# Optimization experiments

Measured on AMD Instinct MI355X. Metric: run time of the kernel, lower is better.

## Reference

```python
import jax, jax.numpy as jnp
import numpy as np

N_NODES = 50000
N_EDGES = 800000
D_IN = 128
D_HID = 128
D_OUT = 2


def setup_inputs() -> dict:
    key = jax.random.key(0)
    ks = jax.random.split(key, 8)
    x = jax.random.normal(ks[0], (N_NODES, D_IN), dtype=jnp.float32)
    edge_index = jax.random.randint(ks[1], (2, N_EDGES), 0, N_NODES, dtype=jnp.int64)
    s = 0.05
    W1_l = jax.random.normal(ks[2], (D_HID, D_IN), dtype=jnp.float32) * s
    W1_r = jax.random.normal(ks[3], (D_HID, D_IN), dtype=jnp.float32) * s
    b1 = jax.random.normal(ks[4], (D_HID,), dtype=jnp.float32) * s
    W2_l = jax.random.normal(ks[5], (D_OUT, D_HID), dtype=jnp.float32) * s
    W2_r = jax.random.normal(ks[6], (D_OUT, D_HID), dtype=jnp.float32) * s
    b2 = jax.random.normal(ks[7], (D_OUT,), dtype=jnp.float32) * s
    return {"x": x, "edge_index": edge_index, "W1_l": W1_l, "W1_r": W1_r,
            "b1": b1, "W2_l": W2_l, "W2_r": W2_r, "b2": b2}


def _sage_conv(x, src, dst, W_l, W_r, b):
    # mean-aggregate neighbor features: gather from src, scatter-sum to dst
    n = x.shape[0]
    msg = x[src]                                            # [E, d]
    agg = jax.ops.segment_sum(msg, dst, num_segments=n)      # [n, d]
    cnt = jax.ops.segment_sum(jnp.ones((src.shape[0],), x.dtype), dst,
                              num_segments=n)
    agg = agg / jnp.maximum(cnt, 1.0)[:, None]
    # lin_l(aggregated) + lin_r(self) + bias  (PyG SAGEConv with root_weight)
    return agg @ W_l.T + x @ W_r.T + b


def reference(x, edge_index, W1_l, W1_r, b1, W2_l, W2_r, b2):
    src, dst = edge_index[0], edge_index[1]
    h = _sage_conv(x, src, dst, W1_l, W1_r, b1)
    h = jax.nn.relu(h)
    out = _sage_conv(h, src, dst, W2_l, W2_r, b2)
    return out
```

## Files before the change

kernel.cpp:

```cpp
#include <hip/hip_runtime.h>

#define N_NODES 50000
#define N_EDGES 800000

typedef __bf16 bf16_8 __attribute__((ext_vector_type(8)));
typedef float  f32_4  __attribute__((ext_vector_type(4)));


__global__ void prep_kernel(const float* __restrict__ W1l, const float* __restrict__ W1r,
                            __bf16* __restrict__ Wt, const float* __restrict__ x,
                            __bf16* __restrict__ xb, int4* __restrict__ deg_p4) {
    int b = blockIdx.x;
    if (b < 3125) {
        int t = b * 256 + threadIdx.x;
        int node = t >> 4, c8 = t & 15;
        const float4* xp = (const float4*)(x + node * 128 + c8 * 8);
        float4 v0 = xp[0], v1 = xp[1];
        bf16_8 o;
        o[0] = (__bf16)v0.x; o[1] = (__bf16)v0.y; o[2] = (__bf16)v0.z; o[3] = (__bf16)v0.w;
        o[4] = (__bf16)v1.x; o[5] = (__bf16)v1.y; o[6] = (__bf16)v1.z; o[7] = (__bf16)v1.w;
        *(bf16_8*)(xb + node * 128 + c8 * 8) = o;
    } else if (b < 3253) {
        int t = (b - 3125) * 256 + threadIdx.x;
        int n = t >> 8, k = t & 255;
        float v = (k < 128) ? W1l[n * 128 + k] : W1r[n * 128 + (k - 128)];
        Wt[t] = (__bf16)v;
    } else {
        int t = (b - 3253) * 256 + threadIdx.x;
        if (t < 200000) deg_p4[t] = make_int4(0, 0, 0, 0);
    }
}

__global__ void deg_pos_kernel(const int* __restrict__ dst, int* __restrict__ deg_p,
                               int* __restrict__ edge_pos) {
    int e = blockIdx.x * 256 + threadIdx.x;
    edge_pos[e] = atomicAdd(&deg_p[dst[e] * 16], 1);
}

__global__ void scan_block_kernel(const int* __restrict__ deg_p, int* __restrict__ rowptr,
                                  int* __restrict__ degc, int* __restrict__ bsum) {
    __shared__ int s[256];
    int i = blockIdx.x * 256 + threadIdx.x;
    int v = (i < N_NODES) ? deg_p[i * 16] : 0;
    if (i < N_NODES) degc[i] = v;
    s[threadIdx.x] = v;
    __syncthreads();
    #pragma unroll
    for (int off = 1; off < 256; off <<= 1) {
        int t = (threadIdx.x >= off) ? s[threadIdx.x - off] : 0;
        __syncthreads();
        s[threadIdx.x] += t;
        __syncthreads();
    }
    if (i < N_NODES) rowptr[i] = s[threadIdx.x] - v;
    if (threadIdx.x == 255) bsum[blockIdx.x] = s[255];
}

__global__ void scan_bsum_kernel(int* __restrict__ bsum) {
    __shared__ int s[256];
    int v = (threadIdx.x < 196) ? bsum[threadIdx.x] : 0;
    s[threadIdx.x] = v;
    __syncthreads();
    #pragma unroll
    for (int off = 1; off < 256; off <<= 1) {
        int t = (threadIdx.x >= off) ? s[threadIdx.x - off] : 0;
        __syncthreads();
        s[threadIdx.x] += t;
        __syncthreads();
    }
    if (threadIdx.x < 196) bsum[threadIdx.x] = s[threadIdx.x] - v;
}

__global__ void fill_csr_kernel(const int* __restrict__ src, const int* __restrict__ dst,
                                const int* __restrict__ rowptr, const int* __restrict__ bsum,
                                const int* __restrict__ edge_pos, int* __restrict__ csr) {
    int e = blockIdx.x * 256 + threadIdx.x;
    int d = dst[e];
    csr[rowptr[d] + bsum[d >> 8] + edge_pos[e]] = src[e];
}

__global__ __launch_bounds__(256) void agg_kernel(
    const int* __restrict__ rowptr, const int* __restrict__ bsum,
    const int* __restrict__ degc, const int* __restrict__ csr,
    const __bf16* __restrict__ xb, __bf16* __restrict__ aggb)
{
    int t = blockIdx.x * 256 + threadIdx.x;
    int node = t >> 4, c8 = t & 15;
    int beg = rowptr[node] + bsum[node >> 8], n = degc[node];
    float acc[8] = {};
    int j = 0;
    for (; j + 2 <= n; j += 2) {
        int s0 = csr[beg + j], s1 = csr[beg + j + 1];
        bf16_8 v0 = *(const bf16_8*)(xb + s0 * 128 + c8 * 8);
        bf16_8 v1 = *(const bf16_8*)(xb + s1 * 128 + c8 * 8);
        #pragma unroll
        for (int u = 0; u < 8; ++u) acc[u] += (float)v0[u] + (float)v1[u];
    }
    if (j < n) {
        int s0 = csr[beg + j];
        bf16_8 v0 = *(const bf16_8*)(xb + s0 * 128 + c8 * 8);
        #pragma unroll
        for (int u = 0; u < 8; ++u) acc[u] += (float)v0[u];
    }
    float inv = 1.0f / fmaxf((float)n, 1.0f);
    bf16_8 o;
    #pragma unroll
    for (int u = 0; u < 8; ++u) o[u] = (__bf16)(acc[u] * inv);
    *(bf16_8*)(aggb + node * 128 + c8 * 8) = o;
}

#define LDA 264
__global__ __launch_bounds__(256) void gemm_fused_kernel(
    const __bf16* __restrict__ aggb, const __bf16* __restrict__ xb,
    const __bf16* __restrict__ Wt, const float* __restrict__ b1,
    const float* __restrict__ W2l, const float* __restrict__ W2r,
    float* __restrict__ y, float* __restrict__ z)
{
    __shared__ __bf16 As[64 * LDA];
    const int i0 = blockIdx.x * 64;
    const int tid = threadIdx.x;

    #pragma unroll
    for (int s = 0; s < 8; ++s) {
        int v = tid + s * 256;
        int row = v >> 5, c8 = v & 31;
        int gi = i0 + row;
        bf16_8 val = {};
        if (gi < N_NODES) {
            val = (c8 < 16) ? *(const bf16_8*)(aggb + gi * 128 + c8 * 8)
                            : *(const bf16_8*)(xb + gi * 128 + (c8 - 16) * 8);
        }
        *(bf16_8*)(&As[row * LDA + c8 * 8]) = val;
    }
    __syncthreads();

    const int wv = tid >> 6, lane = tid & 63;
    const int m0 = wv * 16;
    const int mr = lane & 15, q = lane >> 4;

    f32_4 acc[8];
    #pragma unroll
    for (int nt = 0; nt < 8; ++nt) acc[nt] = (f32_4){0.f, 0.f, 0.f, 0.f};

    #pragma unroll
    for (int ks = 0; ks < 8; ++ks) {
        bf16_8 a = *(const bf16_8*)(&As[(m0 + mr) * LDA + ks * 32 + q * 8]);
        #pragma unroll
        for (int nt = 0; nt < 8; ++nt) {
            bf16_8 b = *(const bf16_8*)(Wt + (nt * 16 + mr) * 256 + ks * 32 + q * 8);
            acc[nt] = __builtin_amdgcn_mfma_f32_16x16x32_bf16(a, b, acc[nt], 0, 0, 0);
        }
    }

    float py0[4] = {}, py1[4] = {}, pz0[4] = {}, pz1[4] = {};
    #pragma unroll
    for (int nt = 0; nt < 8; ++nt) {
        int col = nt * 16 + mr;
        float bb  = b1[col];
        float wl0 = W2l[col], wl1 = W2l[128 + col];
        float wr0 = W2r[col], wr1 = W2r[128 + col];
        #pragma unroll
        for (int r = 0; r < 4; ++r) {
            float hv = fmaxf(acc[nt][r] + bb, 0.f);
            py0[r] += hv * wl0; py1[r] += hv * wl1;
            pz0[r] += hv * wr0; pz1[r] += hv * wr1;
        }
    }
    #pragma unroll
    for (int off = 1; off < 16; off <<= 1) {
        #pragma unroll
        for (int r = 0; r < 4; ++r) {
            py0[r] += __shfl_xor(py0[r], off);
            py1[r] += __shfl_xor(py1[r], off);
            pz0[r] += __shfl_xor(pz0[r], off);
            pz1[r] += __shfl_xor(pz1[r], off);
        }
    }
    if (mr < 4) {
        int r = mr;
        int row = i0 + m0 + q * 4 + r;
        if (row < N_NODES) {
            ((float2*)y)[row] = make_float2(py0[r], py1[r]);
            ((float2*)z)[row] = make_float2(pz0[r], pz1[r]);
        }
    }
}

__global__ void final_kernel(const int* __restrict__ rowptr, const int* __restrict__ bsum,
                             const int* __restrict__ degc, const int* __restrict__ csr,
                             const float* __restrict__ y, const float* __restrict__ z,
                             const float* __restrict__ b2, float* __restrict__ out) {
    int t = blockIdx.x * 256 + threadIdx.x;
    if (t >= 2 * N_NODES) return;
    int node = t >> 1, c = t & 1;
    int beg = rowptr[node] + bsum[node >> 8], n = degc[node];
    float acc = 0.f;
    for (int j = 0; j < n; ++j) acc += y[csr[beg + j] * 2 + c];
    out[t] = acc / fmaxf((float)n, 1.0f) + z[t] + b2[c];
}

extern "C" void kernel_launch(void* const* d_in, const int* in_sizes, int n_in,
                              void* d_out, int out_size, void* d_ws, size_t ws_size,
                              hipStream_t stream) {
    const float* x   = (const float*)d_in[0];
    const int*   ei  = (const int*)  d_in[1];
    const float* W1l = (const float*)d_in[2];
    const float* W1r = (const float*)d_in[3];
    const float* b1  = (const float*)d_in[4];
    const float* W2l = (const float*)d_in[5];
    const float* W2r = (const float*)d_in[6];
    const float* b2  = (const float*)d_in[7];
    float* out = (float*)d_out;
    const int* src = ei;
    const int* dst = ei + N_EDGES;

    char* ws = (char*)d_ws;
    int*    deg_p    = (int*)   (ws + 0);
    int*    edge_pos = (int*)   (ws + 3200000);
    int*    rowptr   = (int*)   (ws + 6400000);
    int*    degc     = (int*)   (ws + 6600192);
    int*    bsum     = (int*)   (ws + 6800384);
    int*    csr      = (int*)   (ws + 6801408);
    __bf16* xb       = (__bf16*)(ws + 10001408);
    __bf16* aggb     = (__bf16*)(ws + 22801408);
    float*  y        = (float*) (ws + 35601408);
    float*  z        = (float*) (ws + 36001408);
    __bf16* Wt       = (__bf16*)(ws + 36401408);

    prep_kernel<<<4035, 256, 0, stream>>>(W1l, W1r, Wt, x, xb, (int4*)deg_p);
    deg_pos_kernel<<<3125, 256, 0, stream>>>(dst, deg_p, edge_pos);
    scan_block_kernel<<<196, 256, 0, stream>>>(deg_p, rowptr, degc, bsum);
    scan_bsum_kernel<<<1, 256, 0, stream>>>(bsum);
    fill_csr_kernel<<<3125, 256, 0, stream>>>(src, dst, rowptr, bsum, edge_pos, csr);
    agg_kernel<<<3125, 256, 0, stream>>>(rowptr, bsum, degc, csr, xb, aggb);
    gemm_fused_kernel<<<782, 256, 0, stream>>>(aggb, xb, Wt, b1, W2l, W2r, y, z);
    final_kernel<<<391, 256, 0, stream>>>(rowptr, bsum, degc, csr, y, z, b2, out);
}
```

Baseline: 213.4 us.

## Fuse all pipeline stages into one persistent cooperative kernel with grid syncs

Replaces the eight separate kernel launches with a single cooperative persistent kernel that runs each stage as a grid-stride loop, separated by grid-wide barriers. Each block redundantly scans the block sums into shared memory instead of running a separate single-block scan kernel. This targets launch overhead and the gaps between small kernels, at the cost of grid.sync latency and reduced parallelism in stages that previously used many more blocks (the grid is capped at 1024 blocks).

```diff
diff --git a/kernel.cpp b/kernel.cpp
--- a/kernel.cpp
+++ b/kernel.cpp
@@ -1,202 +1,220 @@
 #include <hip/hip_runtime.h>
+#include <hip/hip_cooperative_groups.h>
+
+namespace cg = cooperative_groups;
 
 #define N_NODES 50000
 #define N_EDGES 800000
 
 typedef __bf16 bf16_8 __attribute__((ext_vector_type(8)));
 typedef float  f32_4  __attribute__((ext_vector_type(4)));
-
-
-__global__ void prep_kernel(const float* __restrict__ W1l, const float* __restrict__ W1r,
-                            __bf16* __restrict__ Wt, const float* __restrict__ x,
-                            __bf16* __restrict__ xb, int4* __restrict__ deg_p4) {
-    int b = blockIdx.x;
-    if (b < 3125) {
-        int t = b * 256 + threadIdx.x;
+#define LDA 264
+
+
+__global__ __launch_bounds__(256, 4) void mega_kernel(
+    const float* __restrict__ x, const int* __restrict__ src,
+    const int* __restrict__ dst,
+    const float* __restrict__ W1l, const float* __restrict__ W1r,
+    const float* __restrict__ b1,
+    const float* __restrict__ W2l, const float* __restrict__ W2r,
+    const float* __restrict__ b2, float* __restrict__ out,
+    int* __restrict__ deg_p, int* __restrict__ edge_pos,
+    int* __restrict__ rowptr, int* __restrict__ degc, int* __restrict__ bsum,
+    int* __restrict__ csr, __bf16* __restrict__ xb, __bf16* __restrict__ aggb,
+    float* __restrict__ y, float* __restrict__ z, __bf16* __restrict__ Wt)
+{
+    cg::grid_group grid = cg::this_grid();
+    __shared__ char lds[64 * LDA * 2];
+    int*    s_scan = (int*)lds;
+    int*    s_boff = (int*)(lds + 1024);
+    __bf16* As     = (__bf16*)lds;
+
+    const int tid = threadIdx.x;
+    const int g   = blockIdx.x * 256 + tid;
+    const int G   = gridDim.x * 256;
+
+    for (int t = g; t < 800000; t += G) {
         int node = t >> 4, c8 = t & 15;
         const float4* xp = (const float4*)(x + node * 128 + c8 * 8);
         float4 v0 = xp[0], v1 = xp[1];
         bf16_8 o;
         o[0] = (__bf16)v0.x; o[1] = (__bf16)v0.y; o[2] = (__bf16)v0.z; o[3] = (__bf16)v0.w;
         o[4] = (__bf16)v1.x; o[5] = (__bf16)v1.y; o[6] = (__bf16)v1.z; o[7] = (__bf16)v1.w;
-        *(bf16_8*)(xb + node * 128 + c8 * 8) = o;
-    } else if (b < 3253) {
-        int t = (b - 3125) * 256 + threadIdx.x;
+        *(bf16_8*)(xb + t * 8) = o;
+    }
+    for (int t = g; t < 32768; t += G) {
         int n = t >> 8, k = t & 255;
         float v = (k < 128) ? W1l[n * 128 + k] : W1r[n * 128 + (k - 128)];
         Wt[t] = (__bf16)v;
-    } else {
-        int t = (b - 3253) * 256 + threadIdx.x;
-        if (t < 200000) deg_p4[t] = make_int4(0, 0, 0, 0);
-    }
-}
-
-__global__ void deg_pos_kernel(const int* __restrict__ dst, int* __restrict__ deg_p,
-                               int* __restrict__ edge_pos) {
-    int e = blockIdx.x * 256 + threadIdx.x;
-    edge_pos[e] = atomicAdd(&deg_p[dst[e] * 16], 1);
-}
-
-__global__ void scan_block_kernel(const int* __restrict__ deg_p, int* __restrict__ rowptr,
-                                  int* __restrict__ degc, int* __restrict__ bsum) {
-    __shared__ int s[256];
-    int i = blockIdx.x * 256 + threadIdx.x;
-    int v = (i < N_NODES) ? deg_p[i * 16] : 0;
-    if (i < N_NODES) degc[i] = v;
-    s[threadIdx.x] = v;
-    __syncthreads();
-    #pragma unroll
-    for (int off = 1; off < 256; off <<= 1) {
-        int t = (threadIdx.x >= off) ? s[threadIdx.x - off] : 0;
-        __syncthreads();
-        s[threadIdx.x] += t;
-        __syncthreads();
-    }
-    if (i < N_NODES) rowptr[i] = s[threadIdx.x] - v;
-    if (threadIdx.x == 255) bsum[blockIdx.x] = s[255];
-}
-
-__global__ void scan_bsum_kernel(int* __restrict__ bsum) {
-    __shared__ int s[256];
-    int v = (threadIdx.x < 196) ? bsum[threadIdx.x] : 0;
-    s[threadIdx.x] = v;
-    __syncthreads();
-    #pragma unroll
-    for (int off = 1; off < 256; off <<= 1) {
-        int t = (threadIdx.x >= off) ? s[threadIdx.x - off] : 0;
-        __syncthreads();
-        s[threadIdx.x] += t;
-        __syncthreads();
-    }
-    if (threadIdx.x < 196) bsum[threadIdx.x] = s[threadIdx.x] - v;
-}
-
-__global__ void fill_csr_kernel(const int* __restrict__ src, const int* __restrict__ dst,
-                                const int* __restrict__ rowptr, const int* __restrict__ bsum,
-                                const int* __restrict__ edge_pos, int* __restrict__ csr) {
-    int e = blockIdx.x * 256 + threadIdx.x;
-    int d = dst[e];
-    csr[rowptr[d] + bsum[d >> 8] + edge_pos[e]] = src[e];
-}
-
-__global__ __launch_bounds__(256) void agg_kernel(
-    const int* __restrict__ rowptr, const int* __restrict__ bsum,
-    const int* __restrict__ degc, const int* __restrict__ csr,
-    const __bf16* __restrict__ xb, __bf16* __restrict__ aggb)
-{
-    int t = blockIdx.x * 256 + threadIdx.x;
-    int node = t >> 4, c8 = t & 15;
-    int beg = rowptr[node] + bsum[node >> 8], n = degc[node];
-    float acc[8] = {};
-    int j = 0;
-    for (; j + 2 <= n; j += 2) {
-        int s0 = csr[beg + j], s1 = csr[beg + j + 1];
-        bf16_8 v0 = *(const bf16_8*)(xb + s0 * 128 + c8 * 8);
-        bf16_8 v1 = *(const bf16_8*)(xb + s1 * 128 + c8 * 8);
-        #pragma unroll
-        for (int u = 0; u < 8; ++u) acc[u] += (float)v0[u] + (float)v1[u];
-    }
-    if (j < n) {
-        int s0 = csr[beg + j];
-        bf16_8 v0 = *(const bf16_8*)(xb + s0 * 128 + c8 * 8);
-        #pragma unroll
-        for (int u = 0; u < 8; ++u) acc[u] += (float)v0[u];
-    }
-    float inv = 1.0f / fmaxf((float)n, 1.0f);
-    bf16_8 o;
-    #pragma unroll
-    for (int u = 0; u < 8; ++u) o[u] = (__bf16)(acc[u] * inv);
-    *(bf16_8*)(aggb + node * 128 + c8 * 8) = o;
-}
-
-#define LDA 264
-__global__ __launch_bounds__(256) void gemm_fused_kernel(
-    const __bf16* __restrict__ aggb, const __bf16* __restrict__ xb,
-    const __bf16* __restrict__ Wt, const float* __restrict__ b1,
-    const float* __restrict__ W2l, const float* __restrict__ W2r,
-    float* __restrict__ y, float* __restrict__ z)
-{
-    __shared__ __bf16 As[64 * LDA];
-    const int i0 = blockIdx.x * 64;
-    const int tid = threadIdx.x;
-
-    #pragma unroll
-    for (int s = 0; s < 8; ++s) {
-        int v = tid + s * 256;
-        int row = v >> 5, c8 = v & 31;
-        int gi = i0 + row;
-        bf16_8 val = {};
-        if (gi < N_NODES) {
-            val = (c8 < 16) ? *(const bf16_8*)(aggb + gi * 128 + c8 * 8)
-                            : *(const bf16_8*)(xb + gi * 128 + (c8 - 16) * 8);
-        }
-        *(bf16_8*)(&As[row * LDA + c8 * 8]) = val;
-    }
-    __syncthreads();
-
-    const int wv = tid >> 6, lane = tid & 63;
-    const int m0 = wv * 16;
-    const int mr = lane & 15, q = lane >> 4;
-
-    f32_4 acc[8];
-    #pragma unroll
-    for (int nt = 0; nt < 8; ++nt) acc[nt] = (f32_4){0.f, 0.f, 0.f, 0.f};
-
-    #pragma unroll
-    for (int ks = 0; ks < 8; ++ks) {
-        bf16_8 a = *(const bf16_8*)(&As[(m0 + mr) * LDA + ks * 32 + q * 8]);
+    }
+    for (int t = g; t < 200000; t += G)
+        ((int4*)deg_p)[t] = make_int4(0, 0, 0, 0);
+    grid.sync();
+
+    for (int e = g; e < N_EDGES; e += G)
+        edge_pos[e] = atomicAdd(&deg_p[dst[e] * 16], 1);
+    grid.sync();
+
+    for (int vb = blockIdx.x; vb < 196; vb += gridDim.x) {
+        int i = vb * 256 + tid;
+        int v = (i < N_NODES) ? deg_p[i * 16] : 0;
+        if (i < N_NODES) degc[i] = v;
+        s_scan[tid] = v;
+        __syncthreads();
+        #pragma unroll
+        for (int off = 1; off < 256; off <<= 1) {
+            int t2 = (tid >= off) ? s_scan[tid - off] : 0;
+            __syncthreads();
+            s_scan[tid] += t2;
+            __syncthreads();
+        }
+        if (i < N_NODES) rowptr[i] = s_scan[tid] - v;
+        if (tid == 255) bsum[vb] = s_scan[255];
+        __syncthreads();
+    }
+    grid.sync();
+
+    {
+        int v = (tid < 196) ? bsum[tid] : 0;
+        s_scan[tid] = v;
+        __syncthreads();
+        #pragma unroll
+        for (int off = 1; off < 256; off <<= 1) {
+            int t2 = (tid >= off) ? s_scan[tid - off] : 0;
+            __syncthreads();
+            s_scan[tid] += t2;
+            __syncthreads();
+        }
+        s_boff[tid] = s_scan[tid] - v;
+        __syncthreads();
+    }
+
+    for (int e = g; e < N_EDGES; e += G) {
+        int d = dst[e];
+        csr[rowptr[d] + s_boff[d >> 8] + edge_pos[e]] = src[e];
+    }
+    grid.sync();
+
+    for (int t = g; t < 800000; t += G) {
+        int node = t >> 4, c8 = t & 15;
+        int beg = rowptr[node] + s_boff[node >> 8];
+        int n = degc[node];
+        float acc[8] = {};
+        int j = 0;
+        for (; j + 2 <= n; j += 2) {
+            int s0 = csr[beg + j], s1 = csr[beg + j + 1];
+            bf16_8 v0 = *(const bf16_8*)(xb + s0 * 128 + c8 * 8);
+            bf16_8 v1 = *(const bf16_8*)(xb + s1 * 128 + c8 * 8);
+            #pragma unroll
+            for (int u = 0; u < 8; ++u) acc[u] += (float)v0[u] + (float)v1[u];
+        }
+        if (j < n) {
+            int s0 = csr[beg + j];
+            bf16_8 v0 = *(const bf16_8*)(xb + s0 * 128 + c8 * 8);
+            #pragma unroll
+            for (int u = 0; u < 8; ++u) acc[u] += (float)v0[u];
+        }
+        float inv = 1.0f / fmaxf((float)n, 1.0f);
+        bf16_8 o;
+        #pragma unroll
+        for (int u = 0; u < 8; ++u) o[u] = (__bf16)(acc[u] * inv);
+        *(bf16_8*)(aggb + t * 8) = o;
+    }
+    grid.sync();
+
+    for (int tb = blockIdx.x; tb < 782; tb += gridDim.x) {
+        const int i0 = tb * 64;
+        __syncthreads();
+        #pragma unroll
+        for (int s = 0; s < 8; ++s) {
+            int v = tid + s * 256;
+            int row = v >> 5, c8 = v & 31;
+            int gi = i0 + row;
+            bf16_8 val = {};
+            if (gi < N_NODES) {
+                val = (c8 < 16) ? *(const bf16_8*)(aggb + gi * 128 + c8 * 8)
+                                : *(const bf16_8*)(xb + gi * 128 + (c8 - 16) * 8);
+            }
+            *(bf16_8*)(&As[row * LDA + c8 * 8]) = val;
+        }
+        __syncthreads();
+
+        const int wv = tid >> 6, lane = tid & 63;
+        const int m0 = wv * 16;
+        const int mr = lane & 15, q = lane >> 4;
+
+        f32_4 acc[8];
+        #pragma unroll
+        for (int nt = 0; nt < 8; ++nt) acc[nt] = (f32_4){0.f, 0.f, 0.f, 0.f};
+
+        #pragma unroll
+        for (int ks = 0; ks < 8; ++ks) {
+            bf16_8 a = *(const bf16_8*)(&As[(m0 + mr) * LDA + ks * 32 + q * 8]);
+            #pragma unroll
+            for (int nt = 0; nt < 8; ++nt) {
+                bf16_8 b = *(const bf16_8*)(Wt + (nt * 16 + mr) * 256 + ks * 32 + q * 8);
+                acc[nt] = __builtin_amdgcn_mfma_f32_16x16x32_bf16(a, b, acc[nt], 0, 0, 0);
+            }
+        }
+
+        float py0[4] = {}, py1[4] = {}, pz0[4] = {}, pz1[4] = {};
         #pragma unroll
         for (int nt = 0; nt < 8; ++nt) {
-            bf16_8 b = *(const bf16_8*)(Wt + (nt * 16 + mr) * 256 + ks * 32 + q * 8);
-            acc[nt] = __builtin_amdgcn_mfma_f32_16x16x32_bf16(a, b, acc[nt], 0, 0, 0);
-        }
-    }
-
-    float py0[4] = {}, py1[4] = {}, pz0[4] = {}, pz1[4] = {};
-    #pragma unroll
-    for (int nt = 0; nt < 8; ++nt) {
-        int col = nt * 16 + mr;
-        float bb  = b1[col];
-        float wl0 = W2l[col], wl1 = W2l[128 + col];
-        float wr0 = W2r[col], wr1 = W2r[128 + col];
-        #pragma unroll
-        for (int r = 0; r < 4; ++r) {
-            float hv = fmaxf(acc[nt][r] + bb, 0.f);
-            py0[r] += hv * wl0; py1[r] += hv * wl1;
-            pz0[r] += hv * wr0; pz1[r] += hv * wr1;
-        }
-    }
-    #pragma unroll
-    for (int off = 1; off < 16; off <<= 1) {
-        #pragma unroll
-        for (int r = 0; r < 4; ++r) {
-            py0[r] += __shfl_xor(py0[r], off);
-            py1[r] += __shfl_xor(py1[r], off);
-            pz0[r] += __shfl_xor(pz0[r], off);
-            pz1[r] += __shfl_xor(pz1[r], off);
-        }
-    }
-    if (mr < 4) {
-        int r = mr;
-        int row = i0 + m0 + q * 4 + r;
-        if (row < N_NODES) {
-            ((float2*)y)[row] = make_float2(py0[r], py1[r]);
-            ((float2*)z)[row] = make_float2(pz0[r], pz1[r]);
-        }
-    }
-}
-
-__global__ void final_kernel(const int* __restrict__ rowptr, const int* __restrict__ bsum,
-                             const int* __restrict__ degc, const int* __restrict__ csr,
-                             const float* __restrict__ y, const float* __restrict__ z,
-                             const float* __restrict__ b2, float* __restrict__ out) {
-    int t = blockIdx.x * 256 + threadIdx.x;
-    if (t >= 2 * N_NODES) return;
-    int node = t >> 1, c = t & 1;
-    int beg = rowptr[node] + bsum[node >> 8], n = degc[node];
-    float acc = 0.f;
-    for (int j = 0; j < n; ++j) acc += y[csr[beg + j] * 2 + c];
-    out[t] = acc / fmaxf((float)n, 1.0f) + z[t] + b2[c];
+            int col = nt * 16 + mr;
+            float bb  = b1[col];
+            float wl0 = W2l[col], wl1 = W2l[128 + col];
+            float wr0 = W2r[col], wr1 = W2r[128 + col];
+            #pragma unroll
+            for (int r = 0; r < 4; ++r) {
+                float hv = fmaxf(acc[nt][r] + bb, 0.f);
+                py0[r] += hv * wl0; py1[r] += hv * wl1;
+                pz0[r] += hv * wr0; pz1[r] += hv * wr1;
+            }
+        }
+        #pragma unroll
+        for (int off = 1; off < 16; off <<= 1) {
+            #pragma unroll
+            for (int r = 0; r < 4; ++r) {
+                py0[r] += __shfl_xor(py0[r], off);
+                py1[r] += __shfl_xor(py1[r], off);
+                pz0[r] += __shfl_xor(pz0[r], off);
+                pz1[r] += __shfl_xor(pz1[r], off);
+            }
+        }
+        if (mr < 4) {
+            int r = mr;
+            int row = i0 + m0 + q * 4 + r;
+            if (row < N_NODES) {
+                ((float2*)y)[row] = make_float2(py0[r], py1[r]);
+                ((float2*)z)[row] = make_float2(pz0[r], pz1[r]);
+            }
+        }
+    }
+    grid.sync();
+
+    {
+        int v = (tid < 196) ? bsum[tid] : 0;
+        s_scan[tid] = v;
+        __syncthreads();
+        #pragma unroll
+        for (int off = 1; off < 256; off <<= 1) {
+            int t2 = (tid >= off) ? s_scan[tid - off] : 0;
+            __syncthreads();
+            s_scan[tid] += t2;
+            __syncthreads();
+        }
+        s_boff[tid] = s_scan[tid] - v;
+        __syncthreads();
+    }
+
+    for (int t = g; t < 2 * N_NODES; t += G) {
+        int node = t >> 1, c = t & 1;
+        int beg = rowptr[node] + s_boff[node >> 8];
+        int n = degc[node];
+        float acc = 0.f;
+        for (int j = 0; j < n; ++j) acc += y[csr[beg + j] * 2 + c];
+        out[t] = acc / fmaxf((float)n, 1.0f) + z[t] + b2[c];
+    }
 }
 
 extern "C" void kernel_launch(void* const* d_in, const int* in_sizes, int n_in,
@@ -223,16 +241,24 @@
     int*    csr      = (int*)   (ws + 6801408);
     __bf16* xb       = (__bf16*)(ws + 10001408);
     __bf16* aggb     = (__bf16*)(ws + 22801408);
-    float*  y        = (float*) (ws + 35601408);
-    float*  z        = (float*) (ws + 36001408);
+    float*  yb       = (float*) (ws + 35601408);
+    float*  zb       = (float*) (ws + 36001408);
     __bf16* Wt       = (__bf16*)(ws + 36401408);
 
-    prep_kernel<<<4035, 256, 0, stream>>>(W1l, W1r, Wt, x, xb, (int4*)deg_p);
-    deg_pos_kernel<<<3125, 256, 0, stream>>>(dst, deg_p, edge_pos);
-    scan_block_kernel<<<196, 256, 0, stream>>>(deg_p, rowptr, degc, bsum);
-    scan_bsum_kernel<<<1, 256, 0, stream>>>(bsum);
-    fill_csr_kernel<<<3125, 256, 0, stream>>>(src, dst, rowptr, bsum, edge_pos, csr);
-    agg_kernel<<<3125, 256, 0, stream>>>(rowptr, bsum, degc, csr, xb, aggb);
-    gemm_fused_kernel<<<782, 256, 0, stream>>>(aggb, xb, Wt, b1, W2l, W2r, y, z);
-    final_kernel<<<391, 256, 0, stream>>>(rowptr, bsum, degc, csr, y, z, b2, out);
+    int perCU = 0;
+    hipOccupancyMaxActiveBlocksPerMultiprocessor(&perCU, mega_kernel, 256, 0);
+    if (perCU < 1) perCU = 1;
+    int nblk = perCU * 256;
+    if (nblk > 1024) nblk = 1024;
+
+    void* args[] = {
+        (void*)&x, (void*)&src, (void*)&dst,
+        (void*)&W1l, (void*)&W1r, (void*)&b1,
+        (void*)&W2l, (void*)&W2r, (void*)&b2, (void*)&out,
+        (void*)&deg_p, (void*)&edge_pos, (void*)&rowptr, (void*)&degc,
+        (void*)&bsum, (void*)&csr, (void*)&xb, (void*)&aggb,
+        (void*)&yb, (void*)&zb, (void*)&Wt
+    };
+    hipLaunchCooperativeKernel((void*)mega_kernel, dim3(nblk), dim3(256),
+                               args, 0, stream);
 }
```

Measured after the change: 649.9 us. 3.04x slower.

## Fuse degree counting into prep kernel and redundantly scan block sums per block

Applied to the files above, without the earlier changes.

The degree atomic counting moves into the x-to-bf16 conversion kernel, and the zeroing of deg_p becomes a hipMemsetAsync. The single-block scan of the block sums is removed; every block of fill_csr, agg and final now recomputes that 196-entry scan in shared memory. The aggregation loop is unrolled from 2 to 4 neighbors for more memory-level parallelism. This cuts kernel launches and serialization points, at the cost of repeated scan work and barriers in thousands of blocks.

```diff
diff --git a/kernel.cpp b/kernel.cpp
--- a/kernel.cpp
+++ b/kernel.cpp
@@ -7,34 +7,29 @@
 typedef float  f32_4  __attribute__((ext_vector_type(4)));
 
 
-__global__ void prep_kernel(const float* __restrict__ W1l, const float* __restrict__ W1r,
-                            __bf16* __restrict__ Wt, const float* __restrict__ x,
-                            __bf16* __restrict__ xb, int4* __restrict__ deg_p4) {
+__global__ void prep_deg_kernel(const float* __restrict__ W1l, const float* __restrict__ W1r,
+                                __bf16* __restrict__ Wt, const float* __restrict__ x,
+                                __bf16* __restrict__ xb, const int* __restrict__ dst,
+                                int* __restrict__ deg_p, int* __restrict__ edge_pos) {
     int b = blockIdx.x;
     if (b < 3125) {
         int t = b * 256 + threadIdx.x;
+        int d = dst[t];
+        int pos = atomicAdd(&deg_p[d * 16], 1);
         int node = t >> 4, c8 = t & 15;
         const float4* xp = (const float4*)(x + node * 128 + c8 * 8);
         float4 v0 = xp[0], v1 = xp[1];
         bf16_8 o;
         o[0] = (__bf16)v0.x; o[1] = (__bf16)v0.y; o[2] = (__bf16)v0.z; o[3] = (__bf16)v0.w;
         o[4] = (__bf16)v1.x; o[5] = (__bf16)v1.y; o[6] = (__bf16)v1.z; o[7] = (__bf16)v1.w;
-        *(bf16_8*)(xb + node * 128 + c8 * 8) = o;
-    } else if (b < 3253) {
+        *(bf16_8*)(xb + t * 8) = o;
+        edge_pos[t] = pos;
+    } else {
         int t = (b - 3125) * 256 + threadIdx.x;
         int n = t >> 8, k = t & 255;
         float v = (k < 128) ? W1l[n * 128 + k] : W1r[n * 128 + (k - 128)];
         Wt[t] = (__bf16)v;
-    } else {
-        int t = (b - 3253) * 256 + threadIdx.x;
-        if (t < 200000) deg_p4[t] = make_int4(0, 0, 0, 0);
-    }
-}
-
-__global__ void deg_pos_kernel(const int* __restrict__ dst, int* __restrict__ deg_p,
-                               int* __restrict__ edge_pos) {
-    int e = blockIdx.x * 256 + threadIdx.x;
-    edge_pos[e] = atomicAdd(&deg_p[dst[e] * 16], 1);
+    }
 }
 
 __global__ void scan_block_kernel(const int* __restrict__ deg_p, int* __restrict__ rowptr,
@@ -56,27 +51,31 @@
     if (threadIdx.x == 255) bsum[blockIdx.x] = s[255];
 }
 
-__global__ void scan_bsum_kernel(int* __restrict__ bsum) {
-    __shared__ int s[256];
-    int v = (threadIdx.x < 196) ? bsum[threadIdx.x] : 0;
-    s[threadIdx.x] = v;
+__device__ __forceinline__ void local_bsum_scan(const int* __restrict__ bsum,
+                                                int* s_scan, int* s_boff) {
+    int tid = threadIdx.x;
+    int v = (tid < 196) ? bsum[tid] : 0;
+    s_scan[tid] = v;
     __syncthreads();
     #pragma unroll
     for (int off = 1; off < 256; off <<= 1) {
-        int t = (threadIdx.x >= off) ? s[threadIdx.x - off] : 0;
-        __syncthreads();
-        s[threadIdx.x] += t;
-        __syncthreads();
-    }
-    if (threadIdx.x < 196) bsum[threadIdx.x] = s[threadIdx.x] - v;
+        int t = (tid >= off) ? s_scan[tid - off] : 0;
+        __syncthreads();
+        s_scan[tid] += t;
+        __syncthreads();
+    }
+    s_boff[tid] = s_scan[tid] - v;
+    __syncthreads();
 }
 
 __global__ void fill_csr_kernel(const int* __restrict__ src, const int* __restrict__ dst,
                                 const int* __restrict__ rowptr, const int* __restrict__ bsum,
                                 const int* __restrict__ edge_pos, int* __restrict__ csr) {
+    __shared__ int s_scan[256], s_boff[256];
+    local_bsum_scan(bsum, s_scan, s_boff);
     int e = blockIdx.x * 256 + threadIdx.x;
     int d = dst[e];
-    csr[rowptr[d] + bsum[d >> 8] + edge_pos[e]] = src[e];
+    csr[rowptr[d] + s_boff[d >> 8] + edge_pos[e]] = src[e];
 }
 
 __global__ __launch_bounds__(256) void agg_kernel(
@@ -84,19 +83,25 @@
     const int* __restrict__ degc, const int* __restrict__ csr,
     const __bf16* __restrict__ xb, __bf16* __restrict__ aggb)
 {
+    __shared__ int s_scan[256], s_boff[256];
+    local_bsum_scan(bsum, s_scan, s_boff);
     int t = blockIdx.x * 256 + threadIdx.x;
     int node = t >> 4, c8 = t & 15;
-    int beg = rowptr[node] + bsum[node >> 8], n = degc[node];
+    int beg = rowptr[node] + s_boff[node >> 8], n = degc[node];
     float acc[8] = {};
     int j = 0;
-    for (; j + 2 <= n; j += 2) {
-        int s0 = csr[beg + j], s1 = csr[beg + j + 1];
+    for (; j + 4 <= n; j += 4) {
+        int s0 = csr[beg + j],     s1 = csr[beg + j + 1];
+        int s2 = csr[beg + j + 2], s3 = csr[beg + j + 3];
         bf16_8 v0 = *(const bf16_8*)(xb + s0 * 128 + c8 * 8);
         bf16_8 v1 = *(const bf16_8*)(xb + s1 * 128 + c8 * 8);
-        #pragma unroll
-        for (int u = 0; u < 8; ++u) acc[u] += (float)v0[u] + (float)v1[u];
-    }
-    if (j < n) {
+        bf16_8 v2 = *(const bf16_8*)(xb + s2 * 128 + c8 * 8);
+        bf16_8 v3 = *(const bf16_8*)(xb + s3 * 128 + c8 * 8);
+        #pragma unroll
+        for (int u = 0; u < 8; ++u)
+            acc[u] += ((float)v0[u] + (float)v1[u]) + ((float)v2[u] + (float)v3[u]);
+    }
+    for (; j < n; ++j) {
         int s0 = csr[beg + j];
         bf16_8 v0 = *(const bf16_8*)(xb + s0 * 128 + c8 * 8);
         #pragma unroll
@@ -106,7 +111,7 @@
     bf16_8 o;
     #pragma unroll
     for (int u = 0; u < 8; ++u) o[u] = (__bf16)(acc[u] * inv);
-    *(bf16_8*)(aggb + node * 128 + c8 * 8) = o;
+    *(bf16_8*)(aggb + t * 8) = o;
 }
 
 #define LDA 264
@@ -190,10 +195,12 @@
                              const int* __restrict__ degc, const int* __restrict__ csr,
                              const float* __restrict__ y, const float* __restrict__ z,
                              const float* __restrict__ b2, float* __restrict__ out) {
+    __shared__ int s_scan[256], s_boff[256];
+    local_bsum_scan(bsum, s_scan, s_boff);
     int t = blockIdx.x * 256 + threadIdx.x;
     if (t >= 2 * N_NODES) return;
     int node = t >> 1, c = t & 1;
-    int beg = rowptr[node] + bsum[node >> 8], n = degc[node];
+    int beg = rowptr[node] + s_boff[node >> 8], n = degc[node];
     float acc = 0.f;
     for (int j = 0; j < n; ++j) acc += y[csr[beg + j] * 2 + c];
     out[t] = acc / fmaxf((float)n, 1.0f) + z[t] + b2[c];
@@ -227,10 +234,9 @@
     float*  z        = (float*) (ws + 36001408);
     __bf16* Wt       = (__bf16*)(ws + 36401408);
 
-    prep_kernel<<<4035, 256, 0, stream>>>(W1l, W1r, Wt, x, xb, (int4*)deg_p);
-    deg_pos_kernel<<<3125, 256, 0, stream>>>(dst, deg_p, edge_pos);
+    hipMemsetAsync(deg_p, 0, 3200000, stream);
+    prep_deg_kernel<<<3253, 256, 0, stream>>>(W1l, W1r, Wt, x, xb, dst, deg_p, edge_pos);
     scan_block_kernel<<<196, 256, 0, stream>>>(deg_p, rowptr, degc, bsum);
-    scan_bsum_kernel<<<1, 256, 0, stream>>>(bsum);
     fill_csr_kernel<<<3125, 256, 0, stream>>>(src, dst, rowptr, bsum, edge_pos, csr);
     agg_kernel<<<3125, 256, 0, stream>>>(rowptr, bsum, degc, csr, xb, aggb);
     gemm_fused_kernel<<<782, 256, 0, stream>>>(aggb, xb, Wt, b1, W2l, W2r, y, z);
```

Measured after the change: 208.9 us. 2.1% less time.
